# Performance work log

Measured on AMD Instinct MI355X. Metric: run time of the kernel, lower is better.

Reference implementation:

```python
import jax, jax.numpy as jnp
import numpy as np

B, T_OBS, K_PRED, D, U = 1024, 100, 20, 256, 256
T = T_OBS + K_PRED  # len(time_steps) = T_obs + len(time_pred)


def setup_inputs() -> dict:
    key = jax.random.key(0)
    ks = jax.random.split(key, 7)
    latents = jax.random.normal(ks[0], (B, T_OBS, D), dtype=jnp.float32)
    time_steps = jnp.linspace(0.0, 1.0, T, dtype=jnp.float32)
    time_pred = time_steps[-K_PRED:]  # prediction horizon = last K times
    s1 = 1.0 / np.sqrt(D)
    s2 = 1.0 / np.sqrt(U)
    W1 = jax.random.uniform(ks[1], (D, U), jnp.float32, -s1, s1)
    b1 = jax.random.uniform(ks[2], (U,), jnp.float32, -s1, s1)
    W2 = jax.random.uniform(ks[3], (U, U), jnp.float32, -s2, s2)
    b2 = jax.random.uniform(ks[4], (U,), jnp.float32, -s2, s2)
    W3 = jax.random.uniform(ks[5], (U, D), jnp.float32, -s2, s2)
    b3 = jax.random.uniform(ks[6], (D,), jnp.float32, -s2, s2)
    return dict(latents=latents, time_steps=time_steps, time_pred=time_pred,
                W1=W1, b1=b1, W2=W2, b2=b2, W3=W3, b3=b3)


def reference(latents, time_steps, time_pred, W1, b1, W2, b2, W3, b3):
    # ODE-func MLP: latent_dim -> units -> units -> latent_dim (tanh)
    def ode_f(y):
        h = jnp.tanh(y @ W1 + b1)
        h = jnp.tanh(h @ W2 + b2)
        return h @ W3 + b3

    latents_t = jnp.swapaxes(latents, 0, 1)  # [T_obs, B, D]

    # Replicates the original loop semantics exactly: at iteration i the cell
    # integrates from the (prev_t, t_i) left over from iteration i-1 (single
    # Euler step, since every gap < minimum_step = span/50), THEN updates
    # prev_t = t_i, t_i = time_steps[i], and checks membership in time_pred.
    def step(carry, t_next):
        prev_t, t_i, prev_y, j = carry
        yi = prev_y + ode_f(prev_y) * (t_i - prev_t)  # ODECell Euler step
        is_pred = jnp.any(t_next == time_pred)
        j_safe = jnp.clip(j, 0, T_OBS - 1)
        lat_j = jax.lax.dynamic_index_in_dim(latents_t, j_safe, axis=0, keepdims=False)
        prev_y_new = jnp.where(is_pred, yi, lat_j)
        j_new = j + jnp.where(is_pred, 0, 1)
        return (t_i, t_next, prev_y_new, j_new), yi  # Train setting stores yi_ode

    init = (time_steps[0], time_steps[1], latents[:, 0, :], jnp.int32(1))
    _, ys = jax.lax.scan(step, init, time_steps[1:])  # ys: [T-1, B, D]

    new_latents = jnp.concatenate([latents[:, :1, :], jnp.swapaxes(ys, 0, 1)], axis=1)
    return new_latents  # [B, T, D]
```

## Files before the change

kernel.cpp:

```cpp
#include <hip/hip_runtime.h>
#include <hip/hip_bf16.h>

#define NB 1024
#define NTOBS 100
#define NT 120
#define ND 256
#define LAT_BSTRIDE (NTOBS * ND)
#define OUT_BSTRIDE (NT * ND)

#define SEQ_NBLK 64
#define PAR_ROWS 64
#define PAR_BLKS (98 * (NB / PAR_ROWS))

typedef __attribute__((ext_vector_type(8))) short bf16x8;
typedef __attribute__((ext_vector_type(4))) float f32x4;
typedef __attribute__((ext_vector_type(4))) unsigned u32x4;

__device__ __forceinline__ short f2bf(float f) {
    unsigned u = __float_as_uint(f);
    unsigned r = (u + 0x7fffu + ((u >> 16) & 1u)) >> 16;
    return (short)r;
}

__device__ __forceinline__ unsigned cvt_pk_bf16(float lo, float hi) {
    unsigned r;
    asm("v_cvt_pk_bf16_f32 %0, %1, %2" : "=v"(r) : "v"(lo), "v"(hi));
    return r;
}

__device__ __forceinline__ float pade_tanh(float x) {
    float t = fminf(fmaxf(x, -3.0f), 3.0f);
    float t2 = t * t;
    float num = t * (27.0f + t2);
    float den = __builtin_fmaf(9.0f, t2, 27.0f);
    return num * __builtin_amdgcn_rcpf(den);
}

__device__ __forceinline__ int yswz(int r, int c) {
    return (r * 1024 + c * 4) ^ ((r & 7) << 5);
}
__device__ __forceinline__ int aswz(int r, int c) {
    return (r * 512 + c * 2) ^ ((r & 7) << 4);
}
__device__ __forceinline__ int pswz(int r, int c) {
    return (r * 1024 + c * 4) ^ ((r & 15) << 4);
}

__device__ __forceinline__ void gload16(const void* g, void* l) {
    __builtin_amdgcn_global_load_lds(
        (const __attribute__((address_space(1))) void*)g,
        (__attribute__((address_space(3))) void*)l, 16, 0, 0);
}

__global__ void prep_kernel(const float* __restrict__ W1,
                            const float* __restrict__ W2,
                            const float* __restrict__ W3,
                            const float* __restrict__ lat,
                            short* __restrict__ wt,
                            float* __restrict__ out)
{
    int tid = blockIdx.x * blockDim.x + threadIdx.x;
    int nth = gridDim.x * blockDim.x;
    for (int i = tid; i < 65536; i += nth) {
        const int j    = i & 7;
        const int lane = (i >> 3) & 63;
        const int kk   = (i >> 9) & 7;
        const int ct16 = i >> 12;
        const int k = kk * 32 + (lane >> 4) * 8 + j;
        const int n = ct16 * 16 + (lane & 15);
        wt[i]              = f2bf(W1[k * 256 + n]);
        wt[i + 65536]      = f2bf(W2[k * 256 + n]);
        wt[i + 2 * 65536]  = f2bf(W3[k * 256 + n]);
    }
    for (int i = tid; i < NB * ND; i += nth) {
        int b = i >> 8, c = i & 255;
        out[(size_t)b * OUT_BSTRIDE + 0 * ND + c] = lat[(size_t)b * LAT_BSTRIDE + 0 * ND + c];
        out[(size_t)b * OUT_BSTRIDE + 2 * ND + c] = lat[(size_t)b * LAT_BSTRIDE + 1 * ND + c];
    }
}

__global__ __launch_bounds__(512, 2) void ode_main(
    const float* __restrict__ lat, const float* __restrict__ ts,
    const short* __restrict__ wt,
    const float* __restrict__ b1, const float* __restrict__ b2,
    const float* __restrict__ b3, float* __restrict__ out)
{
    __shared__ __align__(16) char smem[98304];

    const int tid = threadIdx.x;
    const int lane = tid & 63, wave = tid >> 6;
    const int l16 = lane & 15, lgr = lane >> 4;
    const short* wt1 = wt;
    const short* wt2 = wt + 65536;
    const short* wt3 = wt + 2 * 65536;

    if (blockIdx.x < SEQ_NBLK) {
        const int b0 = blockIdx.x * 16;
        char* s_y  = smem;
        char* s_h1 = smem + 16384;
        char* s_h2 = smem + 24576;

        bf16x8 w1r[2][8], w2r[2][8], w3r[2][8];
        float bb1[2], bb2[2], bb3[2];
#pragma unroll
        for (int ct = 0; ct < 2; ct++) {
            const int col = wave * 32 + ct * 16 + l16;
            bb1[ct] = b1[col]; bb2[ct] = b2[col]; bb3[ct] = b3[col];
#pragma unroll
            for (int kk = 0; kk < 8; kk++) {
                const int fo = ((wave * 2 + ct) * 8 + kk) * 512 + lane * 8;
                w1r[ct][kk] = *(const bf16x8*)(wt1 + fo);
                w2r[ct][kk] = *(const bf16x8*)(wt2 + fo);
                w3r[ct][kk] = *(const bf16x8*)(wt3 + fo);
            }
        }
        for (int i = tid; i < 16 * 256 / 4; i += 512) {
            const int r = i >> 6, c = (i & 63) * 4;
            f32x4 v = *(const f32x4*)(lat + (size_t)(b0 + r) * LAT_BSTRIDE + 99 * ND + c);
            *(f32x4*)(s_y + yswz(r, c)) = v;
        }
        __syncthreads();

#pragma unroll 1
        for (int step = 0; step < 20; step++) {
            const int k = 100 + step;
            const float dt = ts[k - 1] - ts[k - 2];
            f32x4 acc0, acc1;

            acc0 = (f32x4){0.f, 0.f, 0.f, 0.f};
            acc1 = (f32x4){0.f, 0.f, 0.f, 0.f};
#pragma unroll
            for (int kk = 0; kk < 8; kk++) {
                const int k0 = kk * 32 + lgr * 8;
                f32x4 lo = *(const f32x4*)(s_y + yswz(l16, k0));
                f32x4 hi = *(const f32x4*)(s_y + yswz(l16, k0 + 4));
                u32x4 p;
                p[0] = cvt_pk_bf16(lo[0], lo[1]);
                p[1] = cvt_pk_bf16(lo[2], lo[3]);
                p[2] = cvt_pk_bf16(hi[0], hi[1]);
                p[3] = cvt_pk_bf16(hi[2], hi[3]);
                bf16x8 a = *(bf16x8*)&p;
                acc0 = __builtin_amdgcn_mfma_f32_16x16x32_bf16(a, w1r[0][kk], acc0, 0, 0, 0);
                acc1 = __builtin_amdgcn_mfma_f32_16x16x32_bf16(a, w1r[1][kk], acc1, 0, 0, 0);
            }
#pragma unroll
            for (int ct = 0; ct < 2; ct++) {
                const f32x4 av = ct ? acc1 : acc0;
                const int c = wave * 32 + ct * 16 + l16;
#pragma unroll
                for (int j = 0; j < 4; j++)
                    *(short*)(s_h1 + aswz(lgr * 4 + j, c)) = f2bf(pade_tanh(av[j] + bb1[ct]));
            }
            __syncthreads();

            acc0 = (f32x4){0.f, 0.f, 0.f, 0.f};
            acc1 = (f32x4){0.f, 0.f, 0.f, 0.f};
#pragma unroll
            for (int kk = 0; kk < 8; kk++) {
                const int k0 = kk * 32 + lgr * 8;
                bf16x8 a = *(const bf16x8*)(s_h1 + aswz(l16, k0));
                acc0 = __builtin_amdgcn_mfma_f32_16x16x32_bf16(a, w2r[0][kk], acc0, 0, 0, 0);
                acc1 = __builtin_amdgcn_mfma_f32_16x16x32_bf16(a, w2r[1][kk], acc1, 0, 0, 0);
            }
#pragma unroll
            for (int ct = 0; ct < 2; ct++) {
                const f32x4 av = ct ? acc1 : acc0;
                const int c = wave * 32 + ct * 16 + l16;
#pragma unroll
                for (int j = 0; j < 4; j++)
                    *(short*)(s_h2 + aswz(lgr * 4 + j, c)) = f2bf(pade_tanh(av[j] + bb2[ct]));
            }
            __syncthreads();

            acc0 = (f32x4){0.f, 0.f, 0.f, 0.f};
            acc1 = (f32x4){0.f, 0.f, 0.f, 0.f};
#pragma unroll
            for (int kk = 0; kk < 8; kk++) {
                const int k0 = kk * 32 + lgr * 8;
                bf16x8 a = *(const bf16x8*)(s_h2 + aswz(l16, k0));
                acc0 = __builtin_amdgcn_mfma_f32_16x16x32_bf16(a, w3r[0][kk], acc0, 0, 0, 0);
                acc1 = __builtin_amdgcn_mfma_f32_16x16x32_bf16(a, w3r[1][kk], acc1, 0, 0, 0);
            }
#pragma unroll
            for (int ct = 0; ct < 2; ct++) {
                const f32x4 av = ct ? acc1 : acc0;
                const int c = wave * 32 + ct * 16 + l16;
                const float bcv = ct ? bb3[1] : bb3[0];
#pragma unroll
                for (int j = 0; j < 4; j++) {
                    const int r = lgr * 4 + j;
                    const int yoff = yswz(r, c);
                    const float yold = *(const float*)(s_y + yoff);
                    const float ynew = yold + (av[j] + bcv) * dt;
                    *(float*)(s_y + yoff) = ynew;
                    out[(size_t)(b0 + r) * OUT_BSTRIDE + (size_t)k * ND + c] = ynew;
                }
            }
            __syncthreads();
        }
    } else {
        const int p = blockIdx.x - SEQ_NBLK;
        const int e = p >> 4;
        const int b0 = (p & 15) * PAR_ROWS;
        const int src_t = (e == 0) ? 0 : (e + 1);
        const int out_k = (e == 0) ? 1 : (e + 2);
        const float dt = ts[e + 1] - ts[e];

        char* Af32 = smem;
        char* s_h  = smem + 65536;
        const int rg = wave >> 2, cg = wave & 3;

#pragma unroll
        for (int i = 0; i < 8; i++) {
            const int r = i * 8 + wave;
            const char* src = (const char*)(lat + (size_t)(b0 + r) * LAT_BSTRIDE + (size_t)src_t * ND);
            gload16(src + ((lane * 16) ^ ((r & 15) << 4)), Af32 + r * 1024);
        }
        __syncthreads();

        f32x4 acc[2][4];
        bf16x8 ball[8][4];
        float bc[4];

#pragma unroll
        for (int kk = 0; kk < 8; kk++)
#pragma unroll
            for (int ct = 0; ct < 4; ct++)
                ball[kk][ct] = *(const bf16x8*)(wt1 + ((cg * 4 + ct) * 8 + kk) * 512 + lane * 8);
#pragma unroll
        for (int ct = 0; ct < 4; ct++) bc[ct] = b1[cg * 64 + ct * 16 + l16];
#pragma unroll
        for (int rt = 0; rt < 2; rt++)
#pragma unroll
            for (int ct = 0; ct < 4; ct++) acc[rt][ct] = (f32x4){0.f, 0.f, 0.f, 0.f};
#pragma unroll
        for (int kk = 0; kk < 8; kk++) {
            const int k0 = kk * 32 + lgr * 8;
            bf16x8 a[2];
#pragma unroll
            for (int rt = 0; rt < 2; rt++) {
                const int r = rg * 32 + rt * 16 + l16;
                f32x4 lo = *(const f32x4*)(Af32 + pswz(r, k0));
                f32x4 hi = *(const f32x4*)(Af32 + pswz(r, k0 + 4));
                u32x4 pk;
                pk[0] = cvt_pk_bf16(lo[0], lo[1]);
                pk[1] = cvt_pk_bf16(lo[2], lo[3]);
                pk[2] = cvt_pk_bf16(hi[0], hi[1]);
                pk[3] = cvt_pk_bf16(hi[2], hi[3]);
                a[rt] = *(bf16x8*)&pk;
            }
#pragma unroll
            for (int rt = 0; rt < 2; rt++)
#pragma unroll
                for (int ct = 0; ct < 4; ct++)
                    acc[rt][ct] = __builtin_amdgcn_mfma_f32_16x16x32_bf16(a[rt], ball[kk][ct], acc[rt][ct], 0, 0, 0);
        }
#pragma unroll
        for (int rt = 0; rt < 2; rt++)
#pragma unroll
            for (int ct = 0; ct < 4; ct++) {
                const int c = cg * 64 + ct * 16 + l16;
#pragma unroll
                for (int j = 0; j < 4; j++) {
                    const int r = rg * 32 + rt * 16 + lgr * 4 + j;
                    *(short*)(s_h + aswz(r, c)) = f2bf(pade_tanh(acc[rt][ct][j] + bc[ct]));
                }
            }
        __syncthreads();

#pragma unroll
        for (int kk = 0; kk < 8; kk++)
#pragma unroll
            for (int ct = 0; ct < 4; ct++)
                ball[kk][ct] = *(const bf16x8*)(wt2 + ((cg * 4 + ct) * 8 + kk) * 512 + lane * 8);
#pragma unroll
        for (int ct = 0; ct < 4; ct++) bc[ct] = b2[cg * 64 + ct * 16 + l16];
#pragma unroll
        for (int rt = 0; rt < 2; rt++)
#pragma unroll
            for (int ct = 0; ct < 4; ct++) acc[rt][ct] = (f32x4){0.f, 0.f, 0.f, 0.f};
#pragma unroll
        for (int kk = 0; kk < 8; kk++) {
            const int k0 = kk * 32 + lgr * 8;
            bf16x8 a[2];
#pragma unroll
            for (int rt = 0; rt < 2; rt++)
                a[rt] = *(const bf16x8*)(s_h + aswz(rg * 32 + rt * 16 + l16, k0));
#pragma unroll
            for (int rt = 0; rt < 2; rt++)
#pragma unroll
                for (int ct = 0; ct < 4; ct++)
                    acc[rt][ct] = __builtin_amdgcn_mfma_f32_16x16x32_bf16(a[rt], ball[kk][ct], acc[rt][ct], 0, 0, 0);
        }
        __syncthreads();
#pragma unroll
        for (int rt = 0; rt < 2; rt++)
#pragma unroll
            for (int ct = 0; ct < 4; ct++) {
                const int c = cg * 64 + ct * 16 + l16;
#pragma unroll
                for (int j = 0; j < 4; j++) {
                    const int r = rg * 32 + rt * 16 + lgr * 4 + j;
                    *(short*)(s_h + aswz(r, c)) = f2bf(pade_tanh(acc[rt][ct][j] + bc[ct]));
                }
            }
        __syncthreads();

#pragma unroll
        for (int kk = 0; kk < 8; kk++)
#pragma unroll
            for (int ct = 0; ct < 4; ct++)
                ball[kk][ct] = *(const bf16x8*)(wt3 + ((cg * 4 + ct) * 8 + kk) * 512 + lane * 8);
#pragma unroll
        for (int ct = 0; ct < 4; ct++) bc[ct] = b3[cg * 64 + ct * 16 + l16];
#pragma unroll
        for (int rt = 0; rt < 2; rt++)
#pragma unroll
            for (int ct = 0; ct < 4; ct++) acc[rt][ct] = (f32x4){0.f, 0.f, 0.f, 0.f};
#pragma unroll
        for (int kk = 0; kk < 8; kk++) {
            const int k0 = kk * 32 + lgr * 8;
            bf16x8 a[2];
#pragma unroll
            for (int rt = 0; rt < 2; rt++)
                a[rt] = *(const bf16x8*)(s_h + aswz(rg * 32 + rt * 16 + l16, k0));
#pragma unroll
            for (int rt = 0; rt < 2; rt++)
#pragma unroll
                for (int ct = 0; ct < 4; ct++)
                    acc[rt][ct] = __builtin_amdgcn_mfma_f32_16x16x32_bf16(a[rt], ball[kk][ct], acc[rt][ct], 0, 0, 0);
        }
#pragma unroll
        for (int rt = 0; rt < 2; rt++)
#pragma unroll
            for (int ct = 0; ct < 4; ct++) {
                const int c = cg * 64 + ct * 16 + l16;
#pragma unroll
                for (int j = 0; j < 4; j++) {
                    const int r = rg * 32 + rt * 16 + lgr * 4 + j;
                    const float yold = *(const float*)(Af32 + pswz(r, c));
                    out[(size_t)(b0 + r) * OUT_BSTRIDE + (size_t)out_k * ND + c] =
                        yold + (acc[rt][ct][j] + bc[ct]) * dt;
                }
            }
    }
}

extern "C" void kernel_launch(void* const* d_in, const int* in_sizes, int n_in,
                              void* d_out, int out_size, void* d_ws, size_t ws_size,
                              hipStream_t stream)
{
    const float* lat = (const float*)d_in[0];
    const float* ts  = (const float*)d_in[1];
    const float* W1  = (const float*)d_in[3];
    const float* b1  = (const float*)d_in[4];
    const float* W2  = (const float*)d_in[5];
    const float* b2  = (const float*)d_in[6];
    const float* W3  = (const float*)d_in[7];
    const float* b3  = (const float*)d_in[8];
    float* out = (float*)d_out;
    short* wt = (short*)d_ws;

    hipLaunchKernelGGL(prep_kernel, dim3(2048), dim3(256), 0, stream,
                       W1, W2, W3, lat, wt, out);
    hipLaunchKernelGGL(ode_main, dim3(SEQ_NBLK + PAR_BLKS), dim3(512), 0, stream,
                       lat, ts, wt, b1, b2, b3, out);
}
```

Baseline: 126.6 us.

## Process two tiles per parallel block, prefetching the next tile's latents during compute

Each parallel block now handles two 64-row tiles in sequence instead of one, halving the parallel grid. The next tile's fp32 latents are loaded into LDS asynchronously right after the first layer consumes the current tile, so the load overlaps layers two and three. The old y values are kept in registers so that buffer can be reused. Each wave now owns a 64x32 output slab instead of 32x64, biases are loaded once per block, and lighter LDS-only barriers replace some __syncthreads. The risk is fewer blocks for load balancing alongside the sequential blocks, plus extra register pressure from the held y values.

```diff
diff --git a/kernel.cpp b/kernel.cpp
--- a/kernel.cpp
+++ b/kernel.cpp
@@ -10,7 +10,8 @@
 
 #define SEQ_NBLK 64
 #define PAR_ROWS 64
-#define PAR_BLKS (98 * (NB / PAR_ROWS))
+#define NTILES 1568
+#define PAR_BLKS (NTILES / 2)
 
 typedef __attribute__((ext_vector_type(8))) short bf16x8;
 typedef __attribute__((ext_vector_type(4))) float f32x4;
@@ -50,6 +51,12 @@
     __builtin_amdgcn_global_load_lds(
         (const __attribute__((address_space(1))) void*)g,
         (__attribute__((address_space(3))) void*)l, 16, 0, 0);
+}
+
+__device__ __forceinline__ void lds_barrier() {
+    asm volatile("s_waitcnt lgkmcnt(0)" ::: "memory");
+    __builtin_amdgcn_sched_barrier(0);
+    __builtin_amdgcn_s_barrier();
 }
 
 __global__ void prep_kernel(const float* __restrict__ W1,
@@ -79,6 +86,21 @@
     }
 }
 
+__device__ __forceinline__ void stage_issue(const float* __restrict__ lat,
+                                            int t, char* __restrict__ Af32,
+                                            int wave, int lane)
+{
+    const int e = t >> 4;
+    const int b0 = (t & 15) * 64;
+    const int src_t = (e == 0) ? 0 : (e + 1);
+#pragma unroll
+    for (int i = 0; i < 8; i++) {
+        const int r = i * 8 + wave;
+        const char* src = (const char*)(lat + (size_t)(b0 + r) * LAT_BSTRIDE + (size_t)src_t * ND);
+        gload16(src + ((lane * 16) ^ ((r & 15) << 4)), Af32 + r * 1024);
+    }
+}
+
 __global__ __launch_bounds__(512, 2) void ode_main(
     const float* __restrict__ lat, const float* __restrict__ ts,
     const short* __restrict__ wt,
@@ -199,150 +221,159 @@
             __syncthreads();
         }
     } else {
-        const int p = blockIdx.x - SEQ_NBLK;
-        const int e = p >> 4;
-        const int b0 = (p & 15) * PAR_ROWS;
-        const int src_t = (e == 0) ? 0 : (e + 1);
-        const int out_k = (e == 0) ? 1 : (e + 2);
-        const float dt = ts[e + 1] - ts[e];
-
+        const int t0 = (blockIdx.x - SEQ_NBLK) * 2;
         char* Af32 = smem;
         char* s_h  = smem + 65536;
-        const int rg = wave >> 2, cg = wave & 3;
-
-#pragma unroll
-        for (int i = 0; i < 8; i++) {
-            const int r = i * 8 + wave;
-            const char* src = (const char*)(lat + (size_t)(b0 + r) * LAT_BSTRIDE + (size_t)src_t * ND);
-            gload16(src + ((lane * 16) ^ ((r & 15) << 4)), Af32 + r * 1024);
-        }
+
+        float bb1[2], bb2[2], bb3[2];
+#pragma unroll
+        for (int ct = 0; ct < 2; ct++) {
+            const int c = wave * 32 + ct * 16 + l16;
+            bb1[ct] = b1[c]; bb2[ct] = b2[c]; bb3[ct] = b3[c];
+        }
+
+        stage_issue(lat, t0, Af32, wave, lane);
         __syncthreads();
 
-        f32x4 acc[2][4];
-        bf16x8 ball[8][4];
-        float bc[4];
-
-#pragma unroll
-        for (int kk = 0; kk < 8; kk++)
-#pragma unroll
-            for (int ct = 0; ct < 4; ct++)
-                ball[kk][ct] = *(const bf16x8*)(wt1 + ((cg * 4 + ct) * 8 + kk) * 512 + lane * 8);
-#pragma unroll
-        for (int ct = 0; ct < 4; ct++) bc[ct] = b1[cg * 64 + ct * 16 + l16];
-#pragma unroll
-        for (int rt = 0; rt < 2; rt++)
-#pragma unroll
-            for (int ct = 0; ct < 4; ct++) acc[rt][ct] = (f32x4){0.f, 0.f, 0.f, 0.f};
-#pragma unroll
-        for (int kk = 0; kk < 8; kk++) {
-            const int k0 = kk * 32 + lgr * 8;
-            bf16x8 a[2];
-#pragma unroll
-            for (int rt = 0; rt < 2; rt++) {
-                const int r = rg * 32 + rt * 16 + l16;
-                f32x4 lo = *(const f32x4*)(Af32 + pswz(r, k0));
-                f32x4 hi = *(const f32x4*)(Af32 + pswz(r, k0 + 4));
-                u32x4 pk;
-                pk[0] = cvt_pk_bf16(lo[0], lo[1]);
-                pk[1] = cvt_pk_bf16(lo[2], lo[3]);
-                pk[2] = cvt_pk_bf16(hi[0], hi[1]);
-                pk[3] = cvt_pk_bf16(hi[2], hi[3]);
-                a[rt] = *(bf16x8*)&pk;
-            }
-#pragma unroll
-            for (int rt = 0; rt < 2; rt++)
-#pragma unroll
-                for (int ct = 0; ct < 4; ct++)
-                    acc[rt][ct] = __builtin_amdgcn_mfma_f32_16x16x32_bf16(a[rt], ball[kk][ct], acc[rt][ct], 0, 0, 0);
-        }
-#pragma unroll
-        for (int rt = 0; rt < 2; rt++)
-#pragma unroll
-            for (int ct = 0; ct < 4; ct++) {
-                const int c = cg * 64 + ct * 16 + l16;
-#pragma unroll
-                for (int j = 0; j < 4; j++) {
-                    const int r = rg * 32 + rt * 16 + lgr * 4 + j;
-                    *(short*)(s_h + aswz(r, c)) = f2bf(pade_tanh(acc[rt][ct][j] + bc[ct]));
-                }
-            }
-        __syncthreads();
-
-#pragma unroll
-        for (int kk = 0; kk < 8; kk++)
-#pragma unroll
-            for (int ct = 0; ct < 4; ct++)
-                ball[kk][ct] = *(const bf16x8*)(wt2 + ((cg * 4 + ct) * 8 + kk) * 512 + lane * 8);
-#pragma unroll
-        for (int ct = 0; ct < 4; ct++) bc[ct] = b2[cg * 64 + ct * 16 + l16];
-#pragma unroll
-        for (int rt = 0; rt < 2; rt++)
-#pragma unroll
-            for (int ct = 0; ct < 4; ct++) acc[rt][ct] = (f32x4){0.f, 0.f, 0.f, 0.f};
-#pragma unroll
-        for (int kk = 0; kk < 8; kk++) {
-            const int k0 = kk * 32 + lgr * 8;
-            bf16x8 a[2];
-#pragma unroll
-            for (int rt = 0; rt < 2; rt++)
-                a[rt] = *(const bf16x8*)(s_h + aswz(rg * 32 + rt * 16 + l16, k0));
-#pragma unroll
-            for (int rt = 0; rt < 2; rt++)
-#pragma unroll
-                for (int ct = 0; ct < 4; ct++)
-                    acc[rt][ct] = __builtin_amdgcn_mfma_f32_16x16x32_bf16(a[rt], ball[kk][ct], acc[rt][ct], 0, 0, 0);
-        }
-        __syncthreads();
-#pragma unroll
-        for (int rt = 0; rt < 2; rt++)
-#pragma unroll
-            for (int ct = 0; ct < 4; ct++) {
-                const int c = cg * 64 + ct * 16 + l16;
-#pragma unroll
-                for (int j = 0; j < 4; j++) {
-                    const int r = rg * 32 + rt * 16 + lgr * 4 + j;
-                    *(short*)(s_h + aswz(r, c)) = f2bf(pade_tanh(acc[rt][ct][j] + bc[ct]));
-                }
-            }
-        __syncthreads();
-
-#pragma unroll
-        for (int kk = 0; kk < 8; kk++)
-#pragma unroll
-            for (int ct = 0; ct < 4; ct++)
-                ball[kk][ct] = *(const bf16x8*)(wt3 + ((cg * 4 + ct) * 8 + kk) * 512 + lane * 8);
-#pragma unroll
-        for (int ct = 0; ct < 4; ct++) bc[ct] = b3[cg * 64 + ct * 16 + l16];
-#pragma unroll
-        for (int rt = 0; rt < 2; rt++)
-#pragma unroll
-            for (int ct = 0; ct < 4; ct++) acc[rt][ct] = (f32x4){0.f, 0.f, 0.f, 0.f};
-#pragma unroll
-        for (int kk = 0; kk < 8; kk++) {
-            const int k0 = kk * 32 + lgr * 8;
-            bf16x8 a[2];
-#pragma unroll
-            for (int rt = 0; rt < 2; rt++)
-                a[rt] = *(const bf16x8*)(s_h + aswz(rg * 32 + rt * 16 + l16, k0));
-#pragma unroll
-            for (int rt = 0; rt < 2; rt++)
-#pragma unroll
-                for (int ct = 0; ct < 4; ct++)
-                    acc[rt][ct] = __builtin_amdgcn_mfma_f32_16x16x32_bf16(a[rt], ball[kk][ct], acc[rt][ct], 0, 0, 0);
-        }
-#pragma unroll
-        for (int rt = 0; rt < 2; rt++)
-#pragma unroll
-            for (int ct = 0; ct < 4; ct++) {
-                const int c = cg * 64 + ct * 16 + l16;
-#pragma unroll
-                for (int j = 0; j < 4; j++) {
-                    const int r = rg * 32 + rt * 16 + lgr * 4 + j;
-                    const float yold = *(const float*)(Af32 + pswz(r, c));
-                    out[(size_t)(b0 + r) * OUT_BSTRIDE + (size_t)out_k * ND + c] =
-                        yold + (acc[rt][ct][j] + bc[ct]) * dt;
-                }
-            }
+#pragma unroll 1
+        for (int n = 0; n < 2; n++) {
+            const int t = t0 + n;
+            const int e = t >> 4;
+            const int b0 = (t & 15) * 64;
+            const int out_k = (e == 0) ? 1 : (e + 2);
+            const float dt = ts[e + 1] - ts[e];
+
+            f32x4 acc[4][2];
+            bf16x8 ball[8][2];
+            float yold[4][2][4];
+
+#pragma unroll
+            for (int kk = 0; kk < 8; kk++)
+#pragma unroll
+                for (int ct = 0; ct < 2; ct++)
+                    ball[kk][ct] = *(const bf16x8*)(wt1 + ((wave * 2 + ct) * 8 + kk) * 512 + lane * 8);
+#pragma unroll
+            for (int rt = 0; rt < 4; rt++)
+#pragma unroll
+                for (int ct = 0; ct < 2; ct++) acc[rt][ct] = (f32x4){0.f, 0.f, 0.f, 0.f};
+#pragma unroll
+            for (int kk = 0; kk < 8; kk++) {
+                const int k0 = kk * 32 + lgr * 8;
+                bf16x8 a[4];
+#pragma unroll
+                for (int rt = 0; rt < 4; rt++) {
+                    const int r = rt * 16 + l16;
+                    f32x4 lo = *(const f32x4*)(Af32 + pswz(r, k0));
+                    f32x4 hi = *(const f32x4*)(Af32 + pswz(r, k0 + 4));
+                    u32x4 pk;
+                    pk[0] = cvt_pk_bf16(lo[0], lo[1]);
+                    pk[1] = cvt_pk_bf16(lo[2], lo[3]);
+                    pk[2] = cvt_pk_bf16(hi[0], hi[1]);
+                    pk[3] = cvt_pk_bf16(hi[2], hi[3]);
+                    a[rt] = *(bf16x8*)&pk;
+                }
+#pragma unroll
+                for (int rt = 0; rt < 4; rt++)
+#pragma unroll
+                    for (int ct = 0; ct < 2; ct++)
+                        acc[rt][ct] = __builtin_amdgcn_mfma_f32_16x16x32_bf16(a[rt], ball[kk][ct], acc[rt][ct], 0, 0, 0);
+            }
+#pragma unroll
+            for (int rt = 0; rt < 4; rt++)
+#pragma unroll
+                for (int ct = 0; ct < 2; ct++) {
+                    const int c = wave * 32 + ct * 16 + l16;
+#pragma unroll
+                    for (int j = 0; j < 4; j++)
+                        yold[rt][ct][j] = *(const float*)(Af32 + pswz(rt * 16 + lgr * 4 + j, c));
+                }
+#pragma unroll
+            for (int rt = 0; rt < 4; rt++)
+#pragma unroll
+                for (int ct = 0; ct < 2; ct++) {
+                    const int c = wave * 32 + ct * 16 + l16;
+#pragma unroll
+                    for (int j = 0; j < 4; j++) {
+                        const int r = rt * 16 + lgr * 4 + j;
+                        *(short*)(s_h + aswz(r, c)) = f2bf(pade_tanh(acc[rt][ct][j] + bb1[ct]));
+                    }
+                }
+            lds_barrier();
+
+            if (n == 0) stage_issue(lat, t0 + 1, Af32, wave, lane);
+
+#pragma unroll
+            for (int kk = 0; kk < 8; kk++)
+#pragma unroll
+                for (int ct = 0; ct < 2; ct++)
+                    ball[kk][ct] = *(const bf16x8*)(wt2 + ((wave * 2 + ct) * 8 + kk) * 512 + lane * 8);
+#pragma unroll
+            for (int rt = 0; rt < 4; rt++)
+#pragma unroll
+                for (int ct = 0; ct < 2; ct++) acc[rt][ct] = (f32x4){0.f, 0.f, 0.f, 0.f};
+#pragma unroll
+            for (int kk = 0; kk < 8; kk++) {
+                const int k0 = kk * 32 + lgr * 8;
+                bf16x8 a[4];
+#pragma unroll
+                for (int rt = 0; rt < 4; rt++)
+                    a[rt] = *(const bf16x8*)(s_h + aswz(rt * 16 + l16, k0));
+#pragma unroll
+                for (int rt = 0; rt < 4; rt++)
+#pragma unroll
+                    for (int ct = 0; ct < 2; ct++)
+                        acc[rt][ct] = __builtin_amdgcn_mfma_f32_16x16x32_bf16(a[rt], ball[kk][ct], acc[rt][ct], 0, 0, 0);
+            }
+            lds_barrier();
+#pragma unroll
+            for (int rt = 0; rt < 4; rt++)
+#pragma unroll
+                for (int ct = 0; ct < 2; ct++) {
+                    const int c = wave * 32 + ct * 16 + l16;
+#pragma unroll
+                    for (int j = 0; j < 4; j++) {
+                        const int r = rt * 16 + lgr * 4 + j;
+                        *(short*)(s_h + aswz(r, c)) = f2bf(pade_tanh(acc[rt][ct][j] + bb2[ct]));
+                    }
+                }
+            lds_barrier();
+
+#pragma unroll
+            for (int kk = 0; kk < 8; kk++)
+#pragma unroll
+                for (int ct = 0; ct < 2; ct++)
+                    ball[kk][ct] = *(const bf16x8*)(wt3 + ((wave * 2 + ct) * 8 + kk) * 512 + lane * 8);
+#pragma unroll
+            for (int rt = 0; rt < 4; rt++)
+#pragma unroll
+                for (int ct = 0; ct < 2; ct++) acc[rt][ct] = (f32x4){0.f, 0.f, 0.f, 0.f};
+#pragma unroll
+            for (int kk = 0; kk < 8; kk++) {
+                const int k0 = kk * 32 + lgr * 8;
+                bf16x8 a[4];
+#pragma unroll
+                for (int rt = 0; rt < 4; rt++)
+                    a[rt] = *(const bf16x8*)(s_h + aswz(rt * 16 + l16, k0));
+#pragma unroll
+                for (int rt = 0; rt < 4; rt++)
+#pragma unroll
+                    for (int ct = 0; ct < 2; ct++)
+                        acc[rt][ct] = __builtin_amdgcn_mfma_f32_16x16x32_bf16(a[rt], ball[kk][ct], acc[rt][ct], 0, 0, 0);
+            }
+#pragma unroll
+            for (int rt = 0; rt < 4; rt++)
+#pragma unroll
+                for (int ct = 0; ct < 2; ct++) {
+                    const int c = wave * 32 + ct * 16 + l16;
+#pragma unroll
+                    for (int j = 0; j < 4; j++) {
+                        const int r = rt * 16 + lgr * 4 + j;
+                        out[(size_t)(b0 + r) * OUT_BSTRIDE + (size_t)out_k * ND + c] =
+                            yold[rt][ct][j] + (acc[rt][ct][j] + bb3[ct]) * dt;
+                    }
+                }
+            if (n == 0) __syncthreads();
+        }
     }
 }
 
```

After: 415.1 us. 3.28x slower.
